# Kernel tuning notes

Hardware: AMD Instinct MI355X
Metric: run time of the kernel (lower is better)

## Reference

```python
import jax, jax.numpy as jnp
import numpy as np

B, S, D = 2, 2048, 1024
H, HD, K = 16, 64, 4
F = 4096
EPS = 1e-6
ROPE_BASE = 10000.0
NEG = -1e9


def rmsnorm(x, w):
    return x * jax.lax.rsqrt(jnp.mean(x * x, axis=-1, keepdims=True) + EPS) * w


def rope(t, pos):
    # t: (B,S,H,HD), pos: (B,S,H) per-node position (float)
    inv_freq = 1.0 / (ROPE_BASE ** (jnp.arange(0, HD, 2, dtype=jnp.float32) / HD))
    ang = pos[..., None] * inv_freq  # (B,S,H,HD/2)
    cos, sin = jnp.cos(ang), jnp.sin(ang)
    t1, t2 = t[..., : HD // 2], t[..., HD // 2:]
    return jnp.concatenate([t1 * cos - t2 * sin, t2 * cos + t1 * sin], axis=-1)


def setup_inputs() -> dict:
    key = jax.random.key(0)
    ks = jax.random.split(key, 12)
    s = lambda d: 1.0 / np.sqrt(d)
    return {
        "x": jax.random.normal(ks[0], (B, S, D), jnp.float32),
        "attn_norm_w": jnp.ones((D,), jnp.float32),
        "ffn_norm_w": jnp.ones((D,), jnp.float32),
        "Wq": jax.random.normal(ks[1], (D, H * HD), jnp.float32) * s(D),
        "Wk": jax.random.normal(ks[2], (D, H * HD), jnp.float32) * s(D),
        "Wv": jax.random.normal(ks[3], (D, H * HD), jnp.float32) * s(D),
        "Wo": jax.random.normal(ks[4], (H * HD, D), jnp.float32) * s(H * HD),
        "Wr": jax.random.normal(ks[5], (D, H * K), jnp.float32) * s(D),
        "w1": jax.random.normal(ks[6], (D, F), jnp.float32) * s(D),
        "w2": jax.random.normal(ks[7], (D, F), jnp.float32) * s(D),
        "w3": jax.random.normal(ks[8], (F, D), jnp.float32) * s(F),
    }


def reference(x, attn_norm_w, ffn_norm_w, Wq, Wk, Wv, Wo, Wr, w1, w2, w3):
    # ---- pre-norm + hypergraph node-routed causal attention ----
    h = rmsnorm(x, attn_norm_w)
    # per-(token, head) routing to K hyper-nodes
    logits = (h @ Wr).reshape(B, S, H, K)
    node = jnp.argmax(logits, axis=-1)                      # (B,S,H) int
    onehot = jax.nn.one_hot(node, K, dtype=jnp.float32)     # (B,S,H,K)
    # per-node RoPE position: count of previous same-node tokens
    cum = jnp.cumsum(onehot, axis=1)                        # inclusive
    pos = jnp.take_along_axis(cum, node[..., None], axis=-1)[..., 0] - 1.0  # (B,S,H)

    q = (h @ Wq).reshape(B, S, H, HD)
    k = (h @ Wk).reshape(B, S, H, HD)
    v = (h @ Wv).reshape(B, S, H, HD)
    q = rope(q, pos)
    k = rope(k, pos)

    scores = jnp.einsum("bqhd,bkhd->bhqk", q, k) / np.sqrt(HD)  # (B,H,S,S)
    node_h = jnp.transpose(node, (0, 2, 1))                     # (B,H,S)
    same = node_h[:, :, :, None] == node_h[:, :, None, :]       # intra-node only
    causal = jnp.tril(jnp.ones((S, S), bool))
    allowed = same & causal
    attn = jax.nn.softmax(jnp.where(allowed, scores, NEG), axis=-1)
    ctx = jnp.einsum("bhqk,bkhd->bqhd", attn, v).reshape(B, S, H * HD)
    x = x + ctx @ Wo

    # ---- pre-norm + SwiGLU ----
    h2 = rmsnorm(x, ffn_norm_w)
    ffn = (jax.nn.silu(h2 @ w1) * (h2 @ w2)) @ w3
    return x + ffn
```

## Files before the change

### kernel.cpp

```cpp
#include <hip/hip_runtime.h>
#include <hip/hip_bf16.h>
#include <math.h>

typedef __hip_bfloat16 bf16;

#define B_  2
#define S_  2048
#define D_  1024
#define H_  16
#define HD_ 64
#define KR_ 4
#define F_  4096
#define TOK (B_*S_)
#define NEG (-1.0e9f)

typedef __attribute__((ext_vector_type(8))) short bf16x8_t;
typedef __attribute__((ext_vector_type(4))) float f32x4_t;
typedef unsigned int u32;
#define AS1 __attribute__((address_space(1)))
#define AS3 __attribute__((address_space(3)))

__device__ __forceinline__ float u2f(unsigned short u) {
  union { float f; unsigned int i; } cv; cv.i = ((unsigned int)u) << 16; return cv.f;
}
__device__ __forceinline__ unsigned short f2u(float f) {
  return (unsigned short)(__bfloat16_as_ushort(__float2bfloat16(f)));
}

__device__ __forceinline__ void gl_lds16(const bf16* g, unsigned short* lds_base) {
  __builtin_amdgcn_global_load_lds((const AS1 u32*)g, (AS3 u32*)lds_base, 16, 0, 0);
}

__device__ __forceinline__ float rd1(const void* p, size_t i, bool isbf) {
  return isbf ? __bfloat162float(((const bf16*)p)[i]) : ((const float*)p)[i];
}

__device__ __forceinline__ void xcd_tile(int& bx, int& by) {
  const int nx = gridDim.x;
  const int nwg = nx * gridDim.y;
  const int hw = blockIdx.y * nx + blockIdx.x;
  const int tile = (hw & 7) * (nwg >> 3) + (hw >> 3);
  bx = tile % nx;
  by = tile / nx;
}

#define SWZ_SK8(lane)   (((((lane) & 3) ^ (((lane) >> 3) & 3))) << 3)
#define SWZ_RK(colv)    ((((colv) >> 1) & 3))

__global__ void detect_k(const unsigned* __restrict__ anw_words, int* __restrict__ flag) {
  if (threadIdx.x == 0) *flag = (anw_words[0] == 0x3F803F80u) ? 1 : 0;
}

__global__ __launch_bounds__(256) void transpose_k(const void* W, bf16* __restrict__ WT,
                                                   const int* __restrict__ flagp,
                                                   int K, int N) {
  const bool isbf = (*flagp != 0);
  __shared__ float tile[32][33];
  const int k0 = blockIdx.y * 32, n0 = blockIdx.x * 32;
  const int tid = threadIdx.x;
  const int rl = tid >> 5, cl = tid & 31;
#pragma unroll
  for (int i = 0; i < 4; i++)
    tile[rl + 8 * i][cl] = rd1(W, (size_t)(k0 + rl + 8 * i) * N + n0 + cl, isbf);
  __syncthreads();
#pragma unroll
  for (int i = 0; i < 4; i++)
    WT[(size_t)(n0 + rl + 8 * i) * K + k0 + cl] = __float2bfloat16(tile[cl][rl + 8 * i]);
}

__global__ __launch_bounds__(256) void wrconv_k(const void* Wr, float* __restrict__ Wrf,
                                                const int* __restrict__ flagp) {
  const bool isbf = (*flagp != 0);
  const int i = blockIdx.x * 256 + threadIdx.x;
  Wrf[i] = rd1(Wr, i, isbf);
}

template <bool XDUAL, bool WF>
__global__ __launch_bounds__(256) void rmsnorm_k(const void* x, const void* w,
                                                 bf16* __restrict__ ob,
                                                 float* __restrict__ of,
                                                 const int* __restrict__ flagp) {
  const bool isbf = (*flagp != 0);
  const int row = blockIdx.x;
  const int t = threadIdx.x;
  float v[4];
  float ss = 0.f;
#pragma unroll
  for (int i = 0; i < 4; i++) {
    const size_t idx = (size_t)row * D_ + t + 256 * i;
    v[i] = XDUAL ? rd1(x, idx, isbf) : ((const float*)x)[idx];
    ss += v[i] * v[i];
  }
#pragma unroll
  for (int off = 32; off >= 1; off >>= 1) ss += __shfl_down(ss, off);
  __shared__ float red[4];
  if ((t & 63) == 0) red[t >> 6] = ss;
  __syncthreads();
  const float tot = red[0] + red[1] + red[2] + red[3];
  const float sc = rsqrtf(tot * (1.f / D_) + 1e-6f);
#pragma unroll
  for (int i = 0; i < 4; i++) {
    const int c = t + 256 * i;
    const float r = v[i] * sc * rd1(w, c, isbf);
    ob[(size_t)row * D_ + c] = __float2bfloat16(r);
    if (WF) of[(size_t)row * D_ + c] = r;
  }
}

__global__ __launch_bounds__(256) void router_k(const float* __restrict__ h,
                                                const float* __restrict__ Wrf,
                                                int* __restrict__ node) {
  const int tok0 = blockIdx.x * 16;
  const int t = threadIdx.x;
  __shared__ float hs[16][1024];
  __shared__ float lg[16][64];
  {
    const float4* hsrc = (const float4*)(h + (size_t)tok0 * D_);
    float4* hdst = (float4*)hs;
#pragma unroll
    for (int j = 0; j < 16; j++) hdst[j * 256 + t] = hsrc[j * 256 + t];
  }
  __syncthreads();
  const int col = t & 63, tg = t >> 6;
  float acc[4] = {0.f, 0.f, 0.f, 0.f};
  for (int i = 0; i < D_; i += 4) {
    float wv[4];
#pragma unroll
    for (int u = 0; u < 4; u++) wv[u] = Wrf[(size_t)(i + u) * 64 + col];
#pragma unroll
    for (int tt = 0; tt < 4; tt++) {
      const float4 hv = *(const float4*)&hs[tg * 4 + tt][i];
      acc[tt] = fmaf(hv.x, wv[0], acc[tt]);
      acc[tt] = fmaf(hv.y, wv[1], acc[tt]);
      acc[tt] = fmaf(hv.z, wv[2], acc[tt]);
      acc[tt] = fmaf(hv.w, wv[3], acc[tt]);
    }
  }
#pragma unroll
  for (int tt = 0; tt < 4; tt++) lg[tg * 4 + tt][col] = acc[tt];
  __syncthreads();
  const int tok = t >> 4, hh = t & 15;
  const float* l = &lg[tok][hh * 4];
  float best = l[0];
  int bi = 0;
#pragma unroll
  for (int j = 1; j < KR_; j++) {
    const float vv = l[j];
    if (vv > best) { best = vv; bi = j; }
  }
  node[(size_t)(tok0 + tok) * H_ + hh] = bi;
}

__global__ __launch_bounds__(256) void pos_k(const int* __restrict__ node,
                                             float* __restrict__ pos,
                                             unsigned short* __restrict__ iperm,
                                             unsigned char* __restrict__ gid,
                                             int* __restrict__ gstart) {
  const int bh = blockIdx.x;
  const int b = bh >> 4, h = bh & 15;
  const int t = threadIdx.x;
  __shared__ int sc[256][4];
  int vals[8];
  int c[4] = {0, 0, 0, 0};
#pragma unroll
  for (int i = 0; i < 8; i++) {
    vals[i] = node[(size_t)(b * S_ + t * 8 + i) * H_ + h] & 3;
    c[vals[i]]++;
  }
#pragma unroll
  for (int n = 0; n < 4; n++) sc[t][n] = c[n];
  __syncthreads();
  for (int off = 1; off < 256; off <<= 1) {
    int add[4] = {0, 0, 0, 0};
    if (t >= off) {
#pragma unroll
      for (int n = 0; n < 4; n++) add[n] = sc[t - off][n];
    }
    __syncthreads();
#pragma unroll
    for (int n = 0; n < 4; n++) sc[t][n] += add[n];
    __syncthreads();
  }
  int start[4];
#pragma unroll
  for (int n = 0; n < 4; n++) start[n] = sc[t][n] - c[n];
  int gs[4];
  gs[0] = 0;
  gs[1] = sc[255][0];
  gs[2] = gs[1] + sc[255][1];
  gs[3] = gs[2] + sc[255][2];
  if (t < 4) gstart[bh * 4 + t] = gs[t];
  const size_t bhS = (size_t)bh * S_;
#pragma unroll
  for (int i = 0; i < 8; i++) {
    const int n = vals[i];
    const int rank = start[n]++;
    pos[(size_t)(b * S_ + t * 8 + i) * H_ + h] = (float)rank;
    const int newp = gs[n] + rank;
    iperm[bhS + newp] = (unsigned short)(t * 8 + i);
    gid[bhS + newp] = (unsigned char)n;
  }
}

__global__ __launch_bounds__(512) void rope_k(bf16* __restrict__ q, bf16* __restrict__ k,
                                              const float* __restrict__ pos) {
  const int token = blockIdx.x;
  const int t = threadIdx.x;
  const int h = t >> 5, j = t & 31;
  const float p = pos[token * H_ + h];
  const float inv = exp2f(-(float)j * (13.287712379549449f / 32.f));
  float sn, cs;
  sincosf(p * inv, &sn, &cs);
  const size_t base = (size_t)token * D_ + h * HD_ + j;
  float a = __bfloat162float(q[base]), b = __bfloat162float(q[base + 32]);
  q[base] = __float2bfloat16(a * cs - b * sn);
  q[base + 32] = __float2bfloat16(b * cs + a * sn);
  a = __bfloat162float(k[base]); b = __bfloat162float(k[base + 32]);
  k[base] = __float2bfloat16(a * cs - b * sn);
  k[base + 32] = __float2bfloat16(b * cs + a * sn);
}

__global__ __launch_bounds__(256) void attn_k(const bf16* __restrict__ q,
                                              const bf16* __restrict__ k,
                                              const bf16* __restrict__ v,
                                              const unsigned short* __restrict__ ip,
                                              const unsigned char* __restrict__ gidp,
                                              const int* __restrict__ gstart,
                                              bf16* __restrict__ ctx) {
  const int qt = 31 - blockIdx.x;
  const int h = blockIdx.y;
  const int b = blockIdx.z;
  const int bS = b * S_;
  const int bh = b * H_ + h;
  const size_t bhS = (size_t)bh * S_;
  const int tid = threadIdx.x;
  const int w = tid >> 6;
  const int lane = tid & 63;
  const int col = lane & 15;
  const int quad = lane >> 4;

  __shared__ unsigned short Qs[64][76];
  __shared__ unsigned short Ks[64][76];
  __shared__ unsigned short Vst[64][76];
  __shared__ unsigned short Pa[64][76];

  {
    const int qr = tid & 63, ds = (tid >> 6) * 16;
    const int ipq = ip[bhS + qt * 64 + qr];
    const bf16* src = q + (size_t)(bS + ipq) * D_ + h * HD_ + ds;
#pragma unroll
    for (int i = 0; i < 4; i++)
      *(ushort4*)&Qs[qr][ds + 4 * i] = *(const ushort4*)(src + 4 * i);
  }
  int gq_r[4];
#pragma unroll
  for (int reg = 0; reg < 4; reg++)
    gq_r[reg] = gidp[bhS + qt * 64 + w * 16 + quad * 4 + reg];
  float m_r[4] = {NEG, NEG, NEG, NEG};
  float l_r[4] = {0.f, 0.f, 0.f, 0.f};

  f32x4_t acc_o[4];
#pragma unroll
  for (int ct = 0; ct < 4; ct++) acc_o[ct] = (f32x4_t){0.f, 0.f, 0.f, 0.f};

  const int kt0 = gstart[bh * 4 + gidp[bhS + qt * 64]] >> 6;

  for (int kt = kt0; kt <= qt; kt++) {
    __syncthreads();
    {
      const int key = tid & 63, ds = (tid >> 6) * 16;
      const int ipk = ip[bhS + kt * 64 + key];
      const bf16* ksrc = k + (size_t)(bS + ipk) * D_ + h * HD_ + ds;
      const bf16* vsrc = v + (size_t)(bS + ipk) * D_ + h * HD_ + ds;
#pragma unroll
      for (int i = 0; i < 4; i++) {
        *(ushort4*)&Ks[key][ds + 4 * i] = *(const ushort4*)(ksrc + 4 * i);
        const ushort4 vu = *(const ushort4*)(vsrc + 4 * i);
        Vst[ds + 4 * i + 0][key] = vu.x;
        Vst[ds + 4 * i + 1][key] = vu.y;
        Vst[ds + 4 * i + 2][key] = vu.z;
        Vst[ds + 4 * i + 3][key] = vu.w;
      }
    }
    __syncthreads();

    f32x4_t s[4];
    {
      const bf16x8_t a0 = *(const bf16x8_t*)&Qs[w * 16 + col][quad * 8];
      const bf16x8_t a1 = *(const bf16x8_t*)&Qs[w * 16 + col][32 + quad * 8];
#pragma unroll
      for (int ct = 0; ct < 4; ct++) {
        f32x4_t acc = (f32x4_t){0.f, 0.f, 0.f, 0.f};
        const bf16x8_t b0 = *(const bf16x8_t*)&Ks[ct * 16 + col][quad * 8];
        const bf16x8_t b1 = *(const bf16x8_t*)&Ks[ct * 16 + col][32 + quad * 8];
        acc = __builtin_amdgcn_mfma_f32_16x16x32_bf16(a0, b0, acc, 0, 0, 0);
        acc = __builtin_amdgcn_mfma_f32_16x16x32_bf16(a1, b1, acc, 0, 0, 0);
        s[ct] = acc;
      }
    }
    const bool diag = (kt == qt);
    const size_t kbase = bhS + kt * 64;
    const int gk[4] = {gidp[kbase + col], gidp[kbase + 16 + col],
                       gidp[kbase + 32 + col], gidp[kbase + 48 + col]};
#pragma unroll
    for (int ct = 0; ct < 4; ct++) {
#pragma unroll
      for (int reg = 0; reg < 4; reg++) {
        const int qr = quad * 4 + reg;
        const int kc = ct * 16 + col;
        const bool ok = (gk[ct] == gq_r[reg]) && (!diag || kc <= w * 16 + qr);
        s[ct][reg] = ok ? (s[ct][reg] * 0.125f) : NEG;
      }
    }
    float al[4];
#pragma unroll
    for (int reg = 0; reg < 4; reg++) {
      float tm = fmaxf(fmaxf(s[0][reg], s[1][reg]), fmaxf(s[2][reg], s[3][reg]));
#pragma unroll
      for (int off = 1; off <= 8; off <<= 1) tm = fmaxf(tm, __shfl_xor(tm, off));
      const float mold = m_r[reg];
      const float mnew = fmaxf(mold, tm);
      const bool dead = (mnew <= -5.0e8f);
      const float alpha = dead ? 1.f : __expf(mold - mnew);
      float rowsum = 0.f;
      const int qr = w * 16 + quad * 4 + reg;
#pragma unroll
      for (int ct = 0; ct < 4; ct++) {
        const float e = dead ? 0.f : __expf(s[ct][reg] - mnew);
        rowsum += e;
        Pa[qr][ct * 16 + col] = f2u(e);
      }
#pragma unroll
      for (int off = 1; off <= 8; off <<= 1) rowsum += __shfl_xor(rowsum, off);
      l_r[reg] = l_r[reg] * alpha + rowsum;
      m_r[reg] = mnew;
      al[reg] = alpha;
    }
    {
      const bf16x8_t pa0 = *(const bf16x8_t*)&Pa[w * 16 + col][quad * 8];
      const bf16x8_t pa1 = *(const bf16x8_t*)&Pa[w * 16 + col][32 + quad * 8];
#pragma unroll
      for (int ct = 0; ct < 4; ct++) {
#pragma unroll
        for (int reg = 0; reg < 4; reg++) acc_o[ct][reg] *= al[reg];
        const bf16x8_t b0 = *(const bf16x8_t*)&Vst[ct * 16 + col][quad * 8];
        const bf16x8_t b1 = *(const bf16x8_t*)&Vst[ct * 16 + col][32 + quad * 8];
        acc_o[ct] = __builtin_amdgcn_mfma_f32_16x16x32_bf16(pa0, b0, acc_o[ct], 0, 0, 0);
        acc_o[ct] = __builtin_amdgcn_mfma_f32_16x16x32_bf16(pa1, b1, acc_o[ct], 0, 0, 0);
      }
    }
  }

#pragma unroll
  for (int reg = 0; reg < 4; reg++) {
    const int qr = w * 16 + quad * 4 + reg;
    const int op = ip[bhS + qt * 64 + qr];
    const float l = l_r[reg];
    const float invl = (l > 0.f) ? (1.f / l) : 0.f;
#pragma unroll
    for (int ct = 0; ct < 4; ct++) {
      ctx[(size_t)(bS + op) * D_ + h * HD_ + ct * 16 + col] =
          __float2bfloat16(acc_o[ct][reg] * invl);
    }
  }
}

template <int EPI>
__global__ __launch_bounds__(256) void mgemm_k(const bf16* __restrict__ A,
                                               const bf16* __restrict__ BT,
                                               float* __restrict__ Cf,
                                               void* Cout,
                                               const void* resdual,
                                               const float* __restrict__ resf,
                                               const int* __restrict__ flagp,
                                               int N, int Kd) {
  const bool isbf = (*flagp != 0);
  __shared__ unsigned short As[2][128][32];
  __shared__ unsigned short Bs[2][128][32];
  const int tid = threadIdx.x;
  const int w = tid >> 6, lane = tid & 63;
  const int col = lane & 15, quad = lane >> 4;
  const int wm = w & 1, wn = w >> 1;
  int bx, by;
  xcd_tile(bx, by);
  const int row0 = by * 128, col0 = bx * 128;

  const int srow = lane >> 2, sk8 = SWZ_SK8(lane);
  const bf16* Ag0 = A + (size_t)(row0 + 16 * w + srow) * Kd + sk8;
  const bf16* Ag1 = A + (size_t)(row0 + 64 + 16 * w + srow) * Kd + sk8;
  const bf16* Bg0 = BT + (size_t)(col0 + 16 * w + srow) * Kd + sk8;
  const bf16* Bg1 = BT + (size_t)(col0 + 64 + 16 * w + srow) * Kd + sk8;
  const int rk = SWZ_RK(col);

  f32x4_t acc[4][4];
#pragma unroll
  for (int i = 0; i < 4; i++)
#pragma unroll
    for (int j = 0; j < 4; j++) acc[i][j] = (f32x4_t){0.f, 0.f, 0.f, 0.f};

  gl_lds16(Ag0, &As[0][16 * w][0]);
  gl_lds16(Ag1, &As[0][64 + 16 * w][0]);
  gl_lds16(Bg0, &Bs[0][16 * w][0]);
  gl_lds16(Bg1, &Bs[0][64 + 16 * w][0]);
  __syncthreads();

  int cur = 0;
  for (int kt = 0; kt < Kd; kt += 32) {
    const int nxt = cur ^ 1;
    if (kt + 32 < Kd) {
      gl_lds16(Ag0 + kt + 32, &As[nxt][16 * w][0]);
      gl_lds16(Ag1 + kt + 32, &As[nxt][64 + 16 * w][0]);
      gl_lds16(Bg0 + kt + 32, &Bs[nxt][16 * w][0]);
      gl_lds16(Bg1 + kt + 32, &Bs[nxt][64 + 16 * w][0]);
    }
    bf16x8_t af[4], bfr[4];
#pragma unroll
    for (int i = 0; i < 4; i++) {
      af[i] = *(const bf16x8_t*)&As[cur][wm * 64 + i * 16 + col][(quad ^ rk) * 8];
      bfr[i] = *(const bf16x8_t*)&Bs[cur][wn * 64 + i * 16 + col][(quad ^ rk) * 8];
    }
#pragma unroll
    for (int i = 0; i < 4; i++)
#pragma unroll
      for (int j = 0; j < 4; j++)
        acc[i][j] = __builtin_amdgcn_mfma_f32_16x16x32_bf16(af[i], bfr[j], acc[i][j], 0, 0, 0);
    __syncthreads();
    cur = nxt;
  }

#pragma unroll
  for (int i = 0; i < 4; i++) {
#pragma unroll
    for (int j = 0; j < 4; j++) {
#pragma unroll
      for (int reg = 0; reg < 4; reg++) {
        const int m = row0 + wm * 64 + i * 16 + quad * 4 + reg;
        const int nl = wn * 64 + j * 16 + col;
        if (EPI == 0) {
          const int ng = col0 + nl;
          bf16* base = (bf16*)Cout + (size_t)(ng >> 10) * (TOK * (size_t)D_);
          base[(size_t)m * D_ + (ng & 1023)] = __float2bfloat16(acc[i][j][reg]);
        } else if (EPI == 1) {
          const size_t idx = (size_t)m * N + col0 + nl;
          Cf[idx] = acc[i][j][reg] + rd1(resdual, idx, isbf);
        } else {
          const size_t idx = (size_t)m * N + col0 + nl;
          const float r = acc[i][j][reg] + resf[idx];
          if (isbf) ((bf16*)Cout)[idx] = __float2bfloat16(r);
          else      ((float*)Cout)[idx] = r;
        }
      }
    }
  }
}

template <int EPI>
__global__ __launch_bounds__(256) void mgemm64_k(const bf16* __restrict__ A,
                                                 const bf16* __restrict__ BT,
                                                 float* __restrict__ Cf,
                                                 void* Cout,
                                                 const void* resdual,
                                                 const float* __restrict__ resf,
                                                 const int* __restrict__ flagp,
                                                 int N, int Kd) {
  const bool isbf = (*flagp != 0);
  __shared__ unsigned short As[2][64][32];
  __shared__ unsigned short Bs[2][128][32];
  const int tid = threadIdx.x;
  const int w = tid >> 6, lane = tid & 63;
  const int col = lane & 15, quad = lane >> 4;
  int bx, by;
  xcd_tile(bx, by);
  const int row0 = by * 64, col0 = bx * 128;

  const int srow = lane >> 2, sk8 = SWZ_SK8(lane);
  const bf16* Ag  = A + (size_t)(row0 + 16 * w + srow) * Kd + sk8;
  const bf16* Bg0 = BT + (size_t)(col0 + 32 * w + srow) * Kd + sk8;
  const bf16* Bg1 = BT + (size_t)(col0 + 32 * w + 16 + srow) * Kd + sk8;
  const int rk = SWZ_RK(col);

  f32x4_t acc[4][2];
#pragma unroll
  for (int i = 0; i < 4; i++)
#pragma unroll
    for (int j = 0; j < 2; j++) acc[i][j] = (f32x4_t){0.f, 0.f, 0.f, 0.f};

  gl_lds16(Ag, &As[0][16 * w][0]);
  gl_lds16(Bg0, &Bs[0][32 * w][0]);
  gl_lds16(Bg1, &Bs[0][32 * w + 16][0]);
  __syncthreads();

  int cur = 0;
  for (int kt = 0; kt < Kd; kt += 32) {
    const int nxt = cur ^ 1;
    if (kt + 32 < Kd) {
      gl_lds16(Ag + kt + 32, &As[nxt][16 * w][0]);
      gl_lds16(Bg0 + kt + 32, &Bs[nxt][32 * w][0]);
      gl_lds16(Bg1 + kt + 32, &Bs[nxt][32 * w + 16][0]);
    }
    bf16x8_t af[4], bfr[2];
#pragma unroll
    for (int i = 0; i < 4; i++)
      af[i] = *(const bf16x8_t*)&As[cur][i * 16 + col][(quad ^ rk) * 8];
#pragma unroll
    for (int j = 0; j < 2; j++)
      bfr[j] = *(const bf16x8_t*)&Bs[cur][w * 32 + j * 16 + col][(quad ^ rk) * 8];
#pragma unroll
    for (int i = 0; i < 4; i++)
#pragma unroll
      for (int j = 0; j < 2; j++)
        acc[i][j] = __builtin_amdgcn_mfma_f32_16x16x32_bf16(af[i], bfr[j], acc[i][j], 0, 0, 0);
    __syncthreads();
    cur = nxt;
  }

#pragma unroll
  for (int i = 0; i < 4; i++) {
#pragma unroll
    for (int j = 0; j < 2; j++) {
#pragma unroll
      for (int reg = 0; reg < 4; reg++) {
        const int m = row0 + i * 16 + quad * 4 + reg;
        const int nl = w * 32 + j * 16 + col;
        const size_t idx = (size_t)m * N + col0 + nl;
        if (EPI == 1) {
          Cf[idx] = acc[i][j][reg] + rd1(resdual, idx, isbf);
        } else {
          const float r = acc[i][j][reg] + resf[idx];
          if (isbf) ((bf16*)Cout)[idx] = __float2bfloat16(r);
          else      ((float*)Cout)[idx] = r;
        }
      }
    }
  }
}

__global__ __launch_bounds__(256) void mgate_k(const bf16* __restrict__ A,
                                               const bf16* __restrict__ B1T,
                                               const bf16* __restrict__ B2T,
                                               bf16* __restrict__ G,
                                               int Kd) {
  __shared__ unsigned short As[2][128][32];
  __shared__ unsigned short Bs1[2][64][32];
  __shared__ unsigned short Bs2[2][64][32];
  const int tid = threadIdx.x;
  const int w = tid >> 6, lane = tid & 63;
  const int col = lane & 15, quad = lane >> 4;
  const int wm = w & 1, wn = w >> 1;
  const int hw = blockIdx.y * gridDim.x + blockIdx.x;
  const int rect = hw & 7, inner = hw >> 3;
  const int by = ((rect >> 2) << 4) | (inner >> 4);
  const int bx = ((rect & 3) << 4) | (inner & 15);
  const int row0 = by * 128, col0 = bx * 64;

  const int srow = lane >> 2, sk8 = SWZ_SK8(lane);
  const bf16* Ag0 = A + (size_t)(row0 + 16 * w + srow) * Kd + sk8;
  const bf16* Ag1 = A + (size_t)(row0 + 64 + 16 * w + srow) * Kd + sk8;
  const bf16* B1g = B1T + (size_t)(col0 + 16 * w + srow) * Kd + sk8;
  const bf16* B2g = B2T + (size_t)(col0 + 16 * w + srow) * Kd + sk8;
  const int rk = SWZ_RK(col);

  f32x4_t acc1[4][2], acc2[4][2];
#pragma unroll
  for (int i = 0; i < 4; i++)
#pragma unroll
    for (int j = 0; j < 2; j++) {
      acc1[i][j] = (f32x4_t){0.f, 0.f, 0.f, 0.f};
      acc2[i][j] = (f32x4_t){0.f, 0.f, 0.f, 0.f};
    }

  gl_lds16(Ag0, &As[0][16 * w][0]);
  gl_lds16(Ag1, &As[0][64 + 16 * w][0]);
  gl_lds16(B1g, &Bs1[0][16 * w][0]);
  gl_lds16(B2g, &Bs2[0][16 * w][0]);
  __syncthreads();

  int cur = 0;
  for (int kt = 0; kt < Kd; kt += 32) {
    const int nxt = cur ^ 1;
    if (kt + 32 < Kd) {
      gl_lds16(Ag0 + kt + 32, &As[nxt][16 * w][0]);
      gl_lds16(Ag1 + kt + 32, &As[nxt][64 + 16 * w][0]);
      gl_lds16(B1g + kt + 32, &Bs1[nxt][16 * w][0]);
      gl_lds16(B2g + kt + 32, &Bs2[nxt][16 * w][0]);
    }
    bf16x8_t af[4], b1f[2], b2f[2];
#pragma unroll
    for (int i = 0; i < 4; i++)
      af[i] = *(const bf16x8_t*)&As[cur][wm * 64 + i * 16 + col][(quad ^ rk) * 8];
#pragma unroll
    for (int j = 0; j < 2; j++) {
      b1f[j] = *(const bf16x8_t*)&Bs1[cur][wn * 32 + j * 16 + col][(quad ^ rk) * 8];
      b2f[j] = *(const bf16x8_t*)&Bs2[cur][wn * 32 + j * 16 + col][(quad ^ rk) * 8];
    }
#pragma unroll
    for (int i = 0; i < 4; i++)
#pragma unroll
      for (int j = 0; j < 2; j++) {
        acc1[i][j] = __builtin_amdgcn_mfma_f32_16x16x32_bf16(af[i], b1f[j], acc1[i][j], 0, 0, 0);
        acc2[i][j] = __builtin_amdgcn_mfma_f32_16x16x32_bf16(af[i], b2f[j], acc2[i][j], 0, 0, 0);
      }
    __syncthreads();
    cur = nxt;
  }

#pragma unroll
  for (int i = 0; i < 4; i++) {
#pragma unroll
    for (int j = 0; j < 2; j++) {
#pragma unroll
      for (int reg = 0; reg < 4; reg++) {
        const int m = row0 + wm * 64 + i * 16 + quad * 4 + reg;
        const int n = col0 + wn * 32 + j * 16 + col;
        const float z = acc1[i][j][reg];
        const float sig = 1.f / (1.f + __expf(-z));
        G[(size_t)m * F_ + n] = __float2bfloat16(z * sig * acc2[i][j][reg]);
      }
    }
  }
}

extern "C" void kernel_launch(void* const* d_in, const int* in_sizes, int n_in,
                              void* d_out, int out_size, void* d_ws, size_t ws_size,
                              hipStream_t stream) {
  const void* x   = d_in[0];
  const void* anw = d_in[1];
  const void* fnw = d_in[2];
  const void* Wq  = d_in[3];
  const void* Wk  = d_in[4];
  const void* Wv  = d_in[5];
  const void* Wo  = d_in[6];
  const void* Wr  = d_in[7];
  const void* w1  = d_in[8];
  const void* w2  = d_in[9];
  const void* w3  = d_in[10];

  char* ws = (char*)d_ws;
  int*   node = (int*)ws;
  float* pos  = (float*)(ws + (256 << 10));
  int*   flag = (int*)(ws + (512 << 10));
  unsigned short* iperm = (unsigned short*)(ws + (640u << 10));
  unsigned char*  gidb  = (unsigned char*)(ws + (768u << 10));
  int*   gstart = (int*)(ws + (832u << 10));
  float* x2   = (float*)(ws + (1u << 20));
  bf16*  ctx  = (bf16*)(ws + (17u << 20));
  bf16*  h2   = ctx;
  float* Wrf  = (float*)(ws + (17u << 20));
  char*  r0   = ws + (25u << 20);
  bf16*  hb   = (bf16*)(r0);
  bf16*  qb   = (bf16*)(r0 + (8u << 20));
  bf16*  kb   = (bf16*)(r0 + (16u << 20));
  bf16*  vb   = (bf16*)(r0 + (24u << 20));
  float* hf   = (float*)(r0 + (8u << 20));
  bf16*  g    = (bf16*)(r0);
  bf16*  qkvT = (bf16*)(ws + (57u << 20));
  bf16*  WoT  = (bf16*)(ws + (63u << 20));
  bf16*  w1T  = (bf16*)(ws + (65u << 20));
  bf16*  w2T  = (bf16*)(ws + (73u << 20));
  bf16*  w3T  = (bf16*)(ws + (81u << 20));

  detect_k<<<1, 64, 0, stream>>>((const unsigned*)anw, flag);
  wrconv_k<<<256, 256, 0, stream>>>(Wr, Wrf, flag);
  transpose_k<<<dim3(32, 32), 256, 0, stream>>>(Wq, qkvT,              flag, D_, D_);
  transpose_k<<<dim3(32, 32), 256, 0, stream>>>(Wk, qkvT + (1u << 20), flag, D_, D_);
  transpose_k<<<dim3(32, 32), 256, 0, stream>>>(Wv, qkvT + (2u << 20), flag, D_, D_);
  transpose_k<<<dim3(32, 32), 256, 0, stream>>>(Wo, WoT,               flag, D_, D_);
  transpose_k<<<dim3(128, 32), 256, 0, stream>>>(w1, w1T,              flag, D_, F_);
  transpose_k<<<dim3(128, 32), 256, 0, stream>>>(w2, w2T,              flag, D_, F_);
  transpose_k<<<dim3(32, 128), 256, 0, stream>>>(w3, w3T,              flag, F_, D_);
  rmsnorm_k<true, true><<<TOK, 256, 0, stream>>>(x, anw, hb, hf, flag);
  router_k<<<TOK / 16, 256, 0, stream>>>(hf, Wrf, node);
  pos_k<<<32, 256, 0, stream>>>(node, pos, iperm, gidb, gstart);
  mgemm_k<0><<<dim3(3072 / 128, TOK / 128), 256, 0, stream>>>(hb, qkvT, nullptr, qb, nullptr, nullptr, flag, 3072, D_);
  rope_k<<<TOK, 512, 0, stream>>>(qb, kb, pos);
  attn_k<<<dim3(S_ / 64, H_, B_), 256, 0, stream>>>(qb, kb, vb, iperm, gidb, gstart, ctx);
  mgemm64_k<1><<<dim3(D_ / 128, TOK / 64), 256, 0, stream>>>(ctx, WoT, x2, nullptr, x, nullptr, flag, D_, D_);
  rmsnorm_k<false, false><<<TOK, 256, 0, stream>>>(x2, fnw, h2, nullptr, flag);
  mgate_k<<<dim3(F_ / 64, TOK / 128), 256, 0, stream>>>(h2, w1T, w2T, g, D_);
  mgemm64_k<2><<<dim3(D_ / 128, TOK / 64), 256, 0, stream>>>(g, w3T, nullptr, d_out, nullptr, x2, flag, D_, F_);
}
```

Measured before the change: 493.0 us.

## Fuse weight prep into one kernel, fold RoPE into QKV GEMM, deepen K-step

Merges the dtype-detect, Wr conversion and seven weight-transpose launches into a single prep kernel, dispatching on block index. Applies RoPE in the QKV GEMM epilogue using the per-node positions, which removes the separate rope kernel and its extra read/write pass over q and k. The 64-row GEMM now stages two 32-wide K slices per barrier, halving the number of syncs at the cost of doubled LDS. The RoPE epilogue relies on each warp's 64-column span matching exactly one head.

After: 465.1 us. -5.7%, faster.

```diff
diff --git a/kernel.cpp b/kernel.cpp
--- a/kernel.cpp
+++ b/kernel.cpp
@@ -47,17 +47,32 @@
 #define SWZ_SK8(lane)   (((((lane) & 3) ^ (((lane) >> 3) & 3))) << 3)
 #define SWZ_RK(colv)    ((((colv) >> 1) & 3))
 
-__global__ void detect_k(const unsigned* __restrict__ anw_words, int* __restrict__ flag) {
-  if (threadIdx.x == 0) *flag = (anw_words[0] == 0x3F803F80u) ? 1 : 0;
-}
-
-__global__ __launch_bounds__(256) void transpose_k(const void* W, bf16* __restrict__ WT,
-                                                   const int* __restrict__ flagp,
-                                                   int K, int N) {
-  const bool isbf = (*flagp != 0);
+__global__ __launch_bounds__(256) void prep_k(
+    const void* Wq, const void* Wk, const void* Wv, const void* Wo,
+    const void* w1, const void* w2, const void* w3,
+    bf16* __restrict__ qkvT, bf16* __restrict__ WoT,
+    bf16* __restrict__ w1T, bf16* __restrict__ w2T, bf16* __restrict__ w3T,
+    const void* Wr, float* __restrict__ Wrf,
+    const unsigned* __restrict__ anw_words, int* __restrict__ flag) {
+  const bool isbf = (anw_words[0] == 0x3F803F80u);
+  const int bid = blockIdx.x;
+  const int tid = threadIdx.x;
+  if (bid == 0 && tid == 0) *flag = isbf ? 1 : 0;
+  if (bid >= 16384) {
+    const int i = (bid - 16384) * 256 + tid;
+    Wrf[i] = rd1(Wr, i, isbf);
+    return;
+  }
+  const void* W; bf16* WT; int K, N, nx, local;
+  if (bid < 4096) {
+    const int wi = bid >> 10; local = bid & 1023; K = 1024; N = 1024; nx = 32;
+    W = (wi == 0) ? Wq : (wi == 1) ? Wk : (wi == 2) ? Wv : Wo;
+    WT = (wi == 3) ? WoT : qkvT + ((size_t)wi << 20);
+  } else if (bid < 8192)  { W = w1; WT = w1T; local = bid - 4096;  K = 1024; N = 4096; nx = 128; }
+  else if (bid < 12288)   { W = w2; WT = w2T; local = bid - 8192;  K = 1024; N = 4096; nx = 128; }
+  else                    { W = w3; WT = w3T; local = bid - 12288; K = 4096; N = 1024; nx = 32; }
   __shared__ float tile[32][33];
-  const int k0 = blockIdx.y * 32, n0 = blockIdx.x * 32;
-  const int tid = threadIdx.x;
+  const int n0 = (local % nx) * 32, k0 = (local / nx) * 32;
   const int rl = tid >> 5, cl = tid & 31;
 #pragma unroll
   for (int i = 0; i < 4; i++)
@@ -66,13 +81,6 @@
 #pragma unroll
   for (int i = 0; i < 4; i++)
     WT[(size_t)(n0 + rl + 8 * i) * K + k0 + cl] = __float2bfloat16(tile[cl][rl + 8 * i]);
-}
-
-__global__ __launch_bounds__(256) void wrconv_k(const void* Wr, float* __restrict__ Wrf,
-                                                const int* __restrict__ flagp) {
-  const bool isbf = (*flagp != 0);
-  const int i = blockIdx.x * 256 + threadIdx.x;
-  Wrf[i] = rd1(Wr, i, isbf);
 }
 
 template <bool XDUAL, bool WF>
@@ -200,24 +208,6 @@
     iperm[bhS + newp] = (unsigned short)(t * 8 + i);
     gid[bhS + newp] = (unsigned char)n;
   }
-}
-
-__global__ __launch_bounds__(512) void rope_k(bf16* __restrict__ q, bf16* __restrict__ k,
-                                              const float* __restrict__ pos) {
-  const int token = blockIdx.x;
-  const int t = threadIdx.x;
-  const int h = t >> 5, j = t & 31;
-  const float p = pos[token * H_ + h];
-  const float inv = exp2f(-(float)j * (13.287712379549449f / 32.f));
-  float sn, cs;
-  sincosf(p * inv, &sn, &cs);
-  const size_t base = (size_t)token * D_ + h * HD_ + j;
-  float a = __bfloat162float(q[base]), b = __bfloat162float(q[base + 32]);
-  q[base] = __float2bfloat16(a * cs - b * sn);
-  q[base + 32] = __float2bfloat16(b * cs + a * sn);
-  a = __bfloat162float(k[base]); b = __bfloat162float(k[base + 32]);
-  k[base] = __float2bfloat16(a * cs - b * sn);
-  k[base + 32] = __float2bfloat16(b * cs + a * sn);
 }
 
 __global__ __launch_bounds__(256) void attn_k(const bf16* __restrict__ q,
@@ -372,6 +362,7 @@
                                                void* Cout,
                                                const void* resdual,
                                                const float* __restrict__ resf,
+                                               const float* __restrict__ posp,
                                                const int* __restrict__ flagp,
                                                int N, int Kd) {
   const bool isbf = (*flagp != 0);
@@ -428,26 +419,62 @@
     cur = nxt;
   }
 
-#pragma unroll
-  for (int i = 0; i < 4; i++) {
-#pragma unroll
-    for (int j = 0; j < 4; j++) {
-#pragma unroll
-      for (int reg = 0; reg < 4; reg++) {
-        const int m = row0 + wm * 64 + i * 16 + quad * 4 + reg;
-        const int nl = wn * 64 + j * 16 + col;
-        if (EPI == 0) {
-          const int ng = col0 + nl;
-          bf16* base = (bf16*)Cout + (size_t)(ng >> 10) * (TOK * (size_t)D_);
-          base[(size_t)m * D_ + (ng & 1023)] = __float2bfloat16(acc[i][j][reg]);
-        } else if (EPI == 1) {
+  if (EPI == 0) {
+    const int ng_base = col0 + wn * 64;
+    const int sec = ng_base >> 10;
+    bf16* outp = (bf16*)Cout + (size_t)sec * ((size_t)TOK * D_);
+    if (sec < 2) {
+      const int hh = (ng_base & 1023) >> 6;
+      const float c0 = 13.287712379549449f / 32.f;
+      const float inv0 = exp2f(-(float)col * c0);
+      const float inv1 = exp2f(-(float)(col + 16) * c0);
+#pragma unroll
+      for (int i = 0; i < 4; i++) {
+#pragma unroll
+        for (int reg = 0; reg < 4; reg++) {
+          const int m = row0 + wm * 64 + i * 16 + quad * 4 + reg;
+          const float p = posp[m * H_ + hh];
+          float sn0, cs0, sn1, cs1;
+          sincosf(p * inv0, &sn0, &cs0);
+          sincosf(p * inv1, &sn1, &cs1);
+          const float a0 = acc[i][0][reg], b0 = acc[i][2][reg];
+          const float a1 = acc[i][1][reg], b1 = acc[i][3][reg];
+          bf16* rowp = outp + (size_t)m * D_ + hh * 64;
+          rowp[col]      = __float2bfloat16(a0 * cs0 - b0 * sn0);
+          rowp[col + 32] = __float2bfloat16(b0 * cs0 + a0 * sn0);
+          rowp[col + 16] = __float2bfloat16(a1 * cs1 - b1 * sn1);
+          rowp[col + 48] = __float2bfloat16(b1 * cs1 + a1 * sn1);
+        }
+      }
+    } else {
+#pragma unroll
+      for (int i = 0; i < 4; i++)
+#pragma unroll
+        for (int j = 0; j < 4; j++)
+#pragma unroll
+          for (int reg = 0; reg < 4; reg++) {
+            const int m = row0 + wm * 64 + i * 16 + quad * 4 + reg;
+            const int ng = col0 + wn * 64 + j * 16 + col;
+            outp[(size_t)m * D_ + (ng & 1023)] = __float2bfloat16(acc[i][j][reg]);
+          }
+    }
+  } else {
+#pragma unroll
+    for (int i = 0; i < 4; i++) {
+#pragma unroll
+      for (int j = 0; j < 4; j++) {
+#pragma unroll
+        for (int reg = 0; reg < 4; reg++) {
+          const int m = row0 + wm * 64 + i * 16 + quad * 4 + reg;
+          const int nl = wn * 64 + j * 16 + col;
           const size_t idx = (size_t)m * N + col0 + nl;
-          Cf[idx] = acc[i][j][reg] + rd1(resdual, idx, isbf);
-        } else {
-          const size_t idx = (size_t)m * N + col0 + nl;
-          const float r = acc[i][j][reg] + resf[idx];
-          if (isbf) ((bf16*)Cout)[idx] = __float2bfloat16(r);
-          else      ((float*)Cout)[idx] = r;
+          if (EPI == 1) {
+            Cf[idx] = acc[i][j][reg] + rd1(resdual, idx, isbf);
+          } else {
+            const float r = acc[i][j][reg] + resf[idx];
+            if (isbf) ((bf16*)Cout)[idx] = __float2bfloat16(r);
+            else      ((float*)Cout)[idx] = r;
+          }
         }
       }
     }
@@ -464,8 +491,8 @@
                                                  const int* __restrict__ flagp,
                                                  int N, int Kd) {
   const bool isbf = (*flagp != 0);
-  __shared__ unsigned short As[2][64][32];
-  __shared__ unsigned short Bs[2][128][32];
+  __shared__ unsigned short As[2][2][64][32];
+  __shared__ unsigned short Bs[2][2][128][32];
   const int tid = threadIdx.x;
   const int w = tid >> 6, lane = tid & 63;
   const int col = lane & 15, quad = lane >> 4;
@@ -485,31 +512,37 @@
 #pragma unroll
     for (int j = 0; j < 2; j++) acc[i][j] = (f32x4_t){0.f, 0.f, 0.f, 0.f};
 
-  gl_lds16(Ag, &As[0][16 * w][0]);
-  gl_lds16(Bg0, &Bs[0][32 * w][0]);
-  gl_lds16(Bg1, &Bs[0][32 * w + 16][0]);
+  auto stage = [&](int buf, int kt) {
+#pragma unroll
+    for (int hh = 0; hh < 2; hh++) {
+      gl_lds16(Ag + kt + 32 * hh, &As[buf][hh][16 * w][0]);
+      gl_lds16(Bg0 + kt + 32 * hh, &Bs[buf][hh][32 * w][0]);
+      gl_lds16(Bg1 + kt + 32 * hh, &Bs[buf][hh][32 * w + 16][0]);
+    }
+  };
+
+  stage(0, 0);
   __syncthreads();
 
   int cur = 0;
-  for (int kt = 0; kt < Kd; kt += 32) {
+  for (int kt = 0; kt < Kd; kt += 64) {
     const int nxt = cur ^ 1;
-    if (kt + 32 < Kd) {
-      gl_lds16(Ag + kt + 32, &As[nxt][16 * w][0]);
-      gl_lds16(Bg0 + kt + 32, &Bs[nxt][32 * w][0]);
-      gl_lds16(Bg1 + kt + 32, &Bs[nxt][32 * w + 16][0]);
-    }
-    bf16x8_t af[4], bfr[2];
-#pragma unroll
-    for (int i = 0; i < 4; i++)
-      af[i] = *(const bf16x8_t*)&As[cur][i * 16 + col][(quad ^ rk) * 8];
-#pragma unroll
-    for (int j = 0; j < 2; j++)
-      bfr[j] = *(const bf16x8_t*)&Bs[cur][w * 32 + j * 16 + col][(quad ^ rk) * 8];
-#pragma unroll
-    for (int i = 0; i < 4; i++)
+    if (kt + 64 < Kd) stage(nxt, kt + 64);
+#pragma unroll
+    for (int hh = 0; hh < 2; hh++) {
+      bf16x8_t af[4], bfr[2];
+#pragma unroll
+      for (int i = 0; i < 4; i++)
+        af[i] = *(const bf16x8_t*)&As[cur][hh][i * 16 + col][(quad ^ rk) * 8];
 #pragma unroll
       for (int j = 0; j < 2; j++)
-        acc[i][j] = __builtin_amdgcn_mfma_f32_16x16x32_bf16(af[i], bfr[j], acc[i][j], 0, 0, 0);
+        bfr[j] = *(const bf16x8_t*)&Bs[cur][hh][w * 32 + j * 16 + col][(quad ^ rk) * 8];
+#pragma unroll
+      for (int i = 0; i < 4; i++)
+#pragma unroll
+        for (int j = 0; j < 2; j++)
+          acc[i][j] = __builtin_amdgcn_mfma_f32_16x16x32_bf16(af[i], bfr[j], acc[i][j], 0, 0, 0);
+    }
     __syncthreads();
     cur = nxt;
   }
@@ -659,20 +692,13 @@
   bf16*  w2T  = (bf16*)(ws + (73u << 20));
   bf16*  w3T  = (bf16*)(ws + (81u << 20));
 
-  detect_k<<<1, 64, 0, stream>>>((const unsigned*)anw, flag);
-  wrconv_k<<<256, 256, 0, stream>>>(Wr, Wrf, flag);
-  transpose_k<<<dim3(32, 32), 256, 0, stream>>>(Wq, qkvT,              flag, D_, D_);
-  transpose_k<<<dim3(32, 32), 256, 0, stream>>>(Wk, qkvT + (1u << 20), flag, D_, D_);
-  transpose_k<<<dim3(32, 32), 256, 0, stream>>>(Wv, qkvT + (2u << 20), flag, D_, D_);
-  transpose_k<<<dim3(32, 32), 256, 0, stream>>>(Wo, WoT,               flag, D_, D_);
-  transpose_k<<<dim3(128, 32), 256, 0, stream>>>(w1, w1T,              flag, D_, F_);
-  transpose_k<<<dim3(128, 32), 256, 0, stream>>>(w2, w2T,              flag, D_, F_);
-  transpose_k<<<dim3(32, 128), 256, 0, stream>>>(w3, w3T,              flag, F_, D_);
+  prep_k<<<16640, 256, 0, stream>>>(Wq, Wk, Wv, Wo, w1, w2, w3,
+                                    qkvT, WoT, w1T, w2T, w3T,
+                                    Wr, Wrf, (const unsigned*)anw, flag);
   rmsnorm_k<true, true><<<TOK, 256, 0, stream>>>(x, anw, hb, hf, flag);
   router_k<<<TOK / 16, 256, 0, stream>>>(hf, Wrf, node);
   pos_k<<<32, 256, 0, stream>>>(node, pos, iperm, gidb, gstart);
-  mgemm_k<0><<<dim3(3072 / 128, TOK / 128), 256, 0, stream>>>(hb, qkvT, nullptr, qb, nullptr, nullptr, flag, 3072, D_);
-  rope_k<<<TOK, 512, 0, stream>>>(qb, kb, pos);
+  mgemm_k<0><<<dim3(3072 / 128, TOK / 128), 256, 0, stream>>>(hb, qkvT, nullptr, qb, nullptr, nullptr, pos, flag, 3072, D_);
   attn_k<<<dim3(S_ / 64, H_, B_), 256, 0, stream>>>(qb, kb, vb, iperm, gidb, gstart, ctx);
   mgemm64_k<1><<<dim3(D_ / 128, TOK / 64), 256, 0, stream>>>(ctx, WoT, x2, nullptr, x, nullptr, flag, D_, D_);
   rmsnorm_k<false, false><<<TOK, 256, 0, stream>>>(x2, fnw, h2, nullptr, flag);
```
